# Kernel optimization log

Measured on AMD Instinct MI355X. Metric: run time of the kernel, lower is better.

Reference implementation:

```python
import jax, jax.numpy as jnp
import numpy as np

B, L, D, N, K = 4, 4096, 1024, 64, 3
EPS = 1e-6

def setup_inputs() -> dict:
    key = jax.random.key(0)
    ks = jax.random.split(key, 24)
    f32 = jnp.float32
    inp = {
        'T': jax.random.normal(ks[0], (B, L, D), f32),
        'norm_scale': jnp.ones((D,), f32),
        'in_w': jax.random.normal(ks[1], (2 * D, D), f32) * (1.0 / np.sqrt(D)),
        'in_b': jnp.zeros((2 * D,), f32),
        'dw_w': jax.random.normal(ks[2], (D, 1, K), f32) * (1.0 / np.sqrt(K)),
        'dw_b': jnp.zeros((D,), f32),
        'pw_w': jax.random.normal(ks[3], (D, D), f32) * (1.0 / np.sqrt(D)),
        'pw_b': jnp.zeros((D,), f32),
        'f_win': jax.random.normal(ks[4], (N, D), f32) * (1.0 / np.sqrt(D)),
        'f_wout': jax.random.normal(ks[5], (D, N), f32) * (1.0 / np.sqrt(N)),
        'f_logA': jax.random.normal(ks[6], (N,), f32) * 0.02,
        'f_B': jax.random.normal(ks[7], (N,), f32) * 0.02,
        'f_C': jax.random.normal(ks[8], (N,), f32) * 0.02,
        'f_logdt': jnp.array(0.0, f32),
        'b_win': jax.random.normal(ks[9], (N, D), f32) * (1.0 / np.sqrt(D)),
        'b_wout': jax.random.normal(ks[10], (D, N), f32) * (1.0 / np.sqrt(N)),
        'b_logA': jax.random.normal(ks[11], (N,), f32) * 0.02,
        'b_B': jax.random.normal(ks[12], (N,), f32) * 0.02,
        'b_C': jax.random.normal(ks[13], (N,), f32) * 0.02,
        'b_logdt': jnp.array(0.0, f32),
        'out_w': jax.random.normal(ks[14], (D, D), f32) * (1.0 / np.sqrt(D)),
        'out_b': jnp.zeros((D,), f32),
    }
    return inp

def _ssm(x, win, wout, logA, Bp, Cp, logdt):
    # ZOH discretization of diagonal SSM
    dt = jnp.exp(logdt)
    A = -jnp.exp(logA)
    Abar = jnp.exp(A * dt)
    denom = jnp.where(jnp.abs(A) < EPS, jnp.ones_like(A), A)
    frac = jnp.where(jnp.abs(A) < EPS, dt, (Abar - 1.0) / denom)
    Bbar = frac * Bp
    u = jnp.einsum('bld,nd->bln', x, win)  # (B,L,N)
    h0 = jnp.zeros((x.shape[0], win.shape[0]), x.dtype)
    def step(h, ut):
        h = h * Abar + ut * Bbar
        return h, h * Cp
    _, ys = jax.lax.scan(step, h0, jnp.swapaxes(u, 0, 1))  # (L,B,N)
    y = jnp.swapaxes(ys, 0, 1)
    return jnp.einsum('bln,dn->bld', y, wout)

def reference(T, norm_scale, in_w, in_b, dw_w, dw_b, pw_w, pw_b,
              f_win, f_wout, f_logA, f_B, f_C, f_logdt,
              b_win, b_wout, b_logA, b_B, b_C, b_logdt,
              out_w, out_b):
    # RMSNorm
    rms = jnp.sqrt(jnp.mean(T * T, axis=-1, keepdims=True) + EPS)
    Tn = T / rms * norm_scale
    # in_linear -> chunk
    xz = Tn @ in_w.T + in_b
    x, z = jnp.split(xz, 2, axis=-1)
    gate = jax.nn.sigmoid(z)
    # depthwise-separable conv1d (NCH layout)
    xc = jnp.swapaxes(x, 1, 2)  # (B,D,L)
    xc = jax.lax.conv_general_dilated(
        xc, dw_w, window_strides=(1,), padding=[(K // 2, K // 2)],
        dimension_numbers=('NCH', 'OIH', 'NCH'), feature_group_count=D)
    xc = xc + dw_b[None, :, None]
    xc = jnp.einsum('bdl,ed->bel', xc, pw_w) + pw_b[None, :, None]
    x_conv = jnp.swapaxes(xc, 1, 2)  # (B,L,D)
    # bidirectional SSM
    y_f = _ssm(x_conv, f_win, f_wout, f_logA, f_B, f_C, f_logdt)
    y_b = _ssm(jnp.flip(x_conv, axis=1), b_win, b_wout, b_logA, b_B, b_C, b_logdt)
    y_b = jnp.flip(y_b, axis=1)
    y = (y_f + y_b) * gate
    y = y @ out_w.T + out_b
    return T + y
```

## Files before the change

### kernel.cpp

```cpp
#include <hip/hip_runtime.h>
#include <cstdint>


#define L_SEQ 4096
#define D_DIM 1024
#define B_SZ 4
#define M_TOK (B_SZ * L_SEQ)
#define CHUNKS 64
#define CLEN (L_SEQ / CHUNKS)

typedef short bf16x8 __attribute__((ext_vector_type(8)));
typedef float floatx4 __attribute__((ext_vector_type(4)));

__device__ inline unsigned short f2bf(float f) {
  union { float f; unsigned int u; } v; v.f = f;
  unsigned int r = v.u + 0x7FFFu + ((v.u >> 16) & 1u);
  return (unsigned short)(r >> 16);
}
__device__ inline float bf2f(unsigned short h) {
  union { unsigned int u; float f; } v; v.u = ((unsigned int)h) << 16;
  return v.f;
}

__device__ inline void load_lds16(const unsigned short* g, unsigned short* l) {
  __builtin_amdgcn_global_load_lds(
      (const __attribute__((address_space(1))) unsigned int*)g,
      (__attribute__((address_space(3))) unsigned int*)l, 16, 0, 0);
}

__global__ __launch_bounds__(256) void rmsnorm_kernel(
    const float* __restrict__ T, const float* __restrict__ scale,
    unsigned short* __restrict__ Tn) {
  int tok = blockIdx.x;
  int t = threadIdx.x;
  const float4* row = (const float4*)(T + (size_t)tok * D_DIM);
  float4 v = row[t];
  float ss = v.x*v.x + v.y*v.y + v.z*v.z + v.w*v.w;
  #pragma unroll
  for (int off = 32; off > 0; off >>= 1) ss += __shfl_down(ss, off);
  __shared__ float part[4];
  if ((t & 63) == 0) part[t >> 6] = ss;
  __syncthreads();
  float total = part[0] + part[1] + part[2] + part[3];
  float rinv = rsqrtf(total * (1.0f / D_DIM) + 1e-6f);
  const float4* sc4 = (const float4*)scale;
  float4 s = sc4[t];
  ushort4 o;
  o.x = f2bf(v.x * rinv * s.x); o.y = f2bf(v.y * rinv * s.y);
  o.z = f2bf(v.z * rinv * s.z); o.w = f2bf(v.w * rinv * s.w);
  ((ushort4*)(Tn + (size_t)tok * D_DIM))[t] = o;
}

__global__ __launch_bounds__(256) void f2bf_vec_kernel(
    const float* __restrict__ in, unsigned short* __restrict__ out, int n4) {
  int i = blockIdx.x * 256 + threadIdx.x;
  if (i < n4) {
    float4 v = ((const float4*)in)[i];
    ushort4 o; o.x = f2bf(v.x); o.y = f2bf(v.y); o.z = f2bf(v.z); o.w = f2bf(v.w);
    ((ushort4*)out)[i] = o;
  }
}

__global__ void prepack_kernel(
    const float* __restrict__ f_win, const float* __restrict__ b_win,
    const float* __restrict__ f_wout, const float* __restrict__ b_wout,
    unsigned short* __restrict__ Wu, unsigned short* __restrict__ Wy) {
  int i = blockIdx.x * blockDim.x + threadIdx.x;
  if (i < 128 * D_DIM) {
    int n = i >> 10, k = i & (D_DIM - 1);
    Wu[i] = f2bf((n < 64) ? f_win[n * D_DIM + k] : b_win[(n - 64) * D_DIM + k]);
    int d = i >> 7, kk = i & 127;
    Wy[i] = f2bf((kk < 64) ? f_wout[d * 64 + kk] : b_wout[d * 64 + (kk - 64)]);
  }
}

template<int MODE, typename OUT_T>
__global__ __launch_bounds__(512, 2) void gemm256_kernel(
    const unsigned short* __restrict__ A, const unsigned short* __restrict__ Bw,
    const float* __restrict__ bias, OUT_T* __restrict__ out,
    int M, int N, int Kt,
    const void* __restrict__ aux0, unsigned short* __restrict__ aux1) {
  __shared__ __align__(16) unsigned short As2[2][256 * 64];
  __shared__ __align__(16) unsigned short Bs2[2][256 * 64];
  const int tid = threadIdx.x;
  const int w = tid >> 6, lane = tid & 63;
  const int quad = lane >> 4, lrow = lane & 15;
  const int wm = w >> 2, wn = w & 3;

  const int nx = N >> 8;
  const int nwg = nx * (M >> 8);
  int obid = blockIdx.y * nx + blockIdx.x;
  int swz = (nwg & 7) ? obid : ((obid & 7) * (nwg >> 3) + (obid >> 3));
  const int bm = (swz / nx) << 8;
  const int bn = (swz % nx) << 8;

  const int lr = lane >> 3, ls = lane & 7;
  const int laneOff = lr * Kt + (((ls - lr) & 7) << 3);
  const unsigned short* Asrc = A + (size_t)bm * Kt + laneOff;
  const unsigned short* Bsrc = Bw + (size_t)bn * Kt + laneOff;

  floatx4 acc[8][4] = {};
  const int nkt = Kt >> 6;

  auto stageTile = [&](int buf, int kt) {
    #pragma unroll
    for (int j = 0; j < 4; ++j) {
      int t0 = j * 64 + w * 8;
      load_lds16(Asrc + (size_t)t0 * Kt + kt * 64, &As2[buf][t0 * 64]);
    }
    #pragma unroll
    for (int j = 0; j < 4; ++j) {
      int t0 = j * 64 + w * 8;
      load_lds16(Bsrc + (size_t)t0 * Kt + kt * 64, &Bs2[buf][t0 * 64]);
    }
  };
  auto fragAddr = [&](int r, int ks) {
    return (r << 6) + ((((ks << 2) + quad + r) & 7) << 3);
  };

  const int rA0 = wm * 128 + lrow;
  const int rB0 = wn * 64 + lrow;

  stageTile(0, 0);
  __syncthreads();

  int cur = 0;
  for (int t = 0; t < nkt; ++t) {
    if (t + 1 < nkt) stageTile(cur ^ 1, t + 1);
    const unsigned short* Ab = As2[cur];
    const unsigned short* Bb = Bs2[cur];
    #pragma unroll
    for (int ks = 0; ks < 2; ++ks) {
      bf16x8 af[8], bfr[4];
      #pragma unroll
      for (int mi = 0; mi < 8; ++mi)
        af[mi] = *(const bf16x8*)(Ab + fragAddr(rA0 + mi * 16, ks));
      #pragma unroll
      for (int ni = 0; ni < 4; ++ni)
        bfr[ni] = *(const bf16x8*)(Bb + fragAddr(rB0 + ni * 16, ks));
      __builtin_amdgcn_s_setprio(1);
      #pragma unroll
      for (int mi = 0; mi < 8; ++mi)
        #pragma unroll
        for (int ni = 0; ni < 4; ++ni)
          acc[mi][ni] = __builtin_amdgcn_mfma_f32_16x16x32_bf16(
              af[mi], bfr[ni], acc[mi][ni], 0, 0, 0);
      __builtin_amdgcn_s_setprio(0);
    }
    if (t + 1 < nkt) {
      __syncthreads();
      cur ^= 1;
    }
  }

  #pragma unroll
  for (int mi8 = 0; mi8 < 8; ++mi8) {
    #pragma unroll
    for (int ni = 0; ni < 4; ++ni) {
      #pragma unroll
      for (int r = 0; r < 4; ++r) {
        int m = bm + wm * 128 + mi8 * 16 + quad * 4 + r;
        int n = bn + wn * 64 + ni * 16 + lrow;
        float v = acc[mi8][ni][r];
        if (MODE == 0) {
          if (bias) v += bias[n];
          if (sizeof(OUT_T) == 2) out[(size_t)m * N + n] = (OUT_T)f2bf(v);
          else                    out[(size_t)m * N + n] = (OUT_T)v;
        } else if (MODE == 1) {
          if (bias) v += bias[n];
          if (n < D_DIM) ((unsigned short*)out)[(size_t)m * D_DIM + n] = f2bf(v);
          else aux1[(size_t)m * D_DIM + (n - D_DIM)] = f2bf(1.0f / (1.0f + expf(-v)));
        } else if (MODE == 2) {
          v *= bf2f(((const unsigned short*)aux0)[(size_t)m * N + n]);
          ((unsigned short*)out)[(size_t)m * N + n] = f2bf(v);
        } else {
          if (bias) v += bias[n];
          v += ((const float*)aux0)[(size_t)m * N + n];
          ((float*)out)[(size_t)m * N + n] = v;
        }
      }
    }
  }
}

template<int MODE, typename OUT_T>
__global__ __launch_bounds__(256) void gemm_mfma_kernel(
    const unsigned short* __restrict__ A, const unsigned short* __restrict__ Bw,
    const float* __restrict__ bias, OUT_T* __restrict__ out,
    int M, int N, int Kt,
    const void* __restrict__ aux0, unsigned short* __restrict__ aux1) {
  __shared__ unsigned short As[2][128 * 32];
  __shared__ unsigned short Bs[2][128 * 32];
  int tid = threadIdx.x;
  int wave = tid >> 6, lane = tid & 63;
  int quad = lane >> 4, lrow = lane & 15;
  int bm = blockIdx.y * 128, bn = blockIdx.x * 128;
  int wm = (wave & 1) * 64, wn = (wave >> 1) * 64;

  int r0 = tid >> 2;
  int c8 = (tid & 3) * 8;
  const unsigned short* Ag0 = A  + (size_t)(bm + r0) * Kt + c8;
  const unsigned short* Ag1 = A  + (size_t)(bm + 64 + r0) * Kt + c8;
  const unsigned short* Bg0 = Bw + (size_t)(bn + r0) * Kt + c8;
  const unsigned short* Bg1 = Bw + (size_t)(bn + 64 + r0) * Kt + c8;
  int woff = wave * 512;

  floatx4 acc[4][4] = {};
  int nt = Kt >> 5;

  load_lds16(Ag0, &As[0][0] + woff);
  load_lds16(Ag1, &As[0][0] + 2048 + woff);
  load_lds16(Bg0, &Bs[0][0] + woff);
  load_lds16(Bg1, &Bs[0][0] + 2048 + woff);
  __syncthreads();

  int cur = 0;
  for (int t = 0; t < nt; ++t) {
    if (t + 1 < nt) {
      int k0 = (t + 1) << 5;
      int nb = cur ^ 1;
      load_lds16(Ag0 + k0, &As[nb][0] + woff);
      load_lds16(Ag1 + k0, &As[nb][0] + 2048 + woff);
      load_lds16(Bg0 + k0, &Bs[nb][0] + woff);
      load_lds16(Bg1 + k0, &Bs[nb][0] + 2048 + woff);
    }
    {
      const unsigned short* Ab = &As[cur][0];
      const unsigned short* Bb = &Bs[cur][0];
      bf16x8 af[4], bfr[4];
      #pragma unroll
      for (int mi = 0; mi < 4; ++mi)
        af[mi] = *(const bf16x8*)(Ab + (wm + mi * 16 + lrow) * 32 + quad * 8);
      #pragma unroll
      for (int ni = 0; ni < 4; ++ni)
        bfr[ni] = *(const bf16x8*)(Bb + (wn + ni * 16 + lrow) * 32 + quad * 8);
      __builtin_amdgcn_s_setprio(1);
      #pragma unroll
      for (int mi = 0; mi < 4; ++mi)
        #pragma unroll
        for (int ni = 0; ni < 4; ++ni)
          acc[mi][ni] = __builtin_amdgcn_mfma_f32_16x16x32_bf16(
              af[mi], bfr[ni], acc[mi][ni], 0, 0, 0);
      __builtin_amdgcn_s_setprio(0);
    }
    if (t + 1 < nt) {
      __syncthreads();
      cur ^= 1;
    }
  }

  #pragma unroll
  for (int mi = 0; mi < 4; ++mi) {
    #pragma unroll
    for (int ni = 0; ni < 4; ++ni) {
      #pragma unroll
      for (int r = 0; r < 4; ++r) {
        int m = bm + wm + mi * 16 + quad * 4 + r;
        int n = bn + wn + ni * 16 + lrow;
        float v = acc[mi][ni][r];
        if (MODE == 0) {
          if (bias) v += bias[n];
          if (sizeof(OUT_T) == 2) out[(size_t)m * N + n] = (OUT_T)f2bf(v);
          else                    out[(size_t)m * N + n] = (OUT_T)v;
        } else if (MODE == 1) {
          if (bias) v += bias[n];
          if (n < D_DIM) ((unsigned short*)out)[(size_t)m * D_DIM + n] = f2bf(v);
          else aux1[(size_t)m * D_DIM + (n - D_DIM)] = f2bf(1.0f / (1.0f + expf(-v)));
        } else if (MODE == 2) {
          v *= bf2f(((const unsigned short*)aux0)[(size_t)m * N + n]);
          ((unsigned short*)out)[(size_t)m * N + n] = f2bf(v);
        } else {
          if (bias) v += bias[n];
          v += ((const float*)aux0)[(size_t)m * N + n];
          ((float*)out)[(size_t)m * N + n] = v;
        }
      }
    }
  }
}

__global__ __launch_bounds__(256) void dwconv_kernel(
    const unsigned short* __restrict__ x, const float* __restrict__ w,
    const float* __restrict__ b, unsigned short* __restrict__ out) {
  size_t i8 = (size_t)blockIdx.x * 256 + threadIdx.x;
  int d8 = (int)(i8 & (D_DIM / 8 - 1));
  size_t tok = i8 >> 7;
  int l = (int)(tok & (L_SEQ - 1));
  int d0 = d8 * 8;
  size_t base = tok * D_DIM + d0;
  bf16x8 cur = *(const bf16x8*)(x + base);
  float acc[8];
  #pragma unroll
  for (int j = 0; j < 8; ++j) {
    int d = d0 + j;
    acc[j] = b[d] + w[d * 3 + 1] * bf2f((unsigned short)cur[j]);
  }
  if (l > 0) {
    bf16x8 prv = *(const bf16x8*)(x + base - D_DIM);
    #pragma unroll
    for (int j = 0; j < 8; ++j) acc[j] += w[(d0 + j) * 3 + 0] * bf2f((unsigned short)prv[j]);
  }
  if (l < L_SEQ - 1) {
    bf16x8 nxt = *(const bf16x8*)(x + base + D_DIM);
    #pragma unroll
    for (int j = 0; j < 8; ++j) acc[j] += w[(d0 + j) * 3 + 2] * bf2f((unsigned short)nxt[j]);
  }
  bf16x8 o;
  #pragma unroll
  for (int j = 0; j < 8; ++j) o[j] = (short)f2bf(acc[j]);
  *(bf16x8*)(out + base) = o;
}

__device__ inline void ssm_params(
    int col,
    const float* f_logA, const float* f_B, const float* f_C, const float* f_logdt,
    const float* b_logA, const float* b_B, const float* b_C, const float* b_logdt,
    float& Abar, float& Bbar, float& Cc, float& Aa, float& dt) {
  int dir = col >> 6, n = col & 63;
  const float* logA  = dir ? b_logA  : f_logA;
  const float* Bp    = dir ? b_B     : f_B;
  const float* Cp    = dir ? b_C     : f_C;
  const float* logdt = dir ? b_logdt : f_logdt;
  dt = expf(logdt[0]);
  Aa = -expf(logA[n]);
  Abar = expf(Aa * dt);
  float frac = (fabsf(Aa) < 1e-6f) ? dt : (Abar - 1.0f) / Aa;
  Bbar = frac * Bp[n];
  Cc = Cp[n];
}

__global__ __launch_bounds__(128) void scan_s1_kernel(
    const float* __restrict__ u, float* __restrict__ states,
    const float* __restrict__ f_logA, const float* __restrict__ f_B,
    const float* __restrict__ f_C, const float* __restrict__ f_logdt,
    const float* __restrict__ b_logA, const float* __restrict__ b_B,
    const float* __restrict__ b_C, const float* __restrict__ b_logdt) {
  int col = threadIdx.x;
  int chunk = blockIdx.x, b = blockIdx.y;
  float Abar, Bbar, Cc, Aa, dt;
  ssm_params(col, f_logA, f_B, f_C, f_logdt, b_logA, b_B, b_C, b_logdt,
             Abar, Bbar, Cc, Aa, dt);
  size_t base = ((size_t)b * L_SEQ + (size_t)chunk * CLEN) * 128 + col;
  float h = 0.0f;
  if (col < 64) {
    for (int i0 = 0; i0 < CLEN; i0 += 8) {
      float uv[8];
      #pragma unroll
      for (int j = 0; j < 8; ++j) uv[j] = u[base + (size_t)(i0 + j) * 128];
      #pragma unroll
      for (int j = 0; j < 8; ++j) h = h * Abar + uv[j] * Bbar;
    }
  } else {
    for (int i0 = CLEN - 1; i0 >= 0; i0 -= 8) {
      float uv[8];
      #pragma unroll
      for (int j = 0; j < 8; ++j) uv[j] = u[base + (size_t)(i0 - j) * 128];
      #pragma unroll
      for (int j = 0; j < 8; ++j) h = h * Abar + uv[j] * Bbar;
    }
  }
  states[((size_t)b * CHUNKS + chunk) * 128 + col] = h;
}

__global__ __launch_bounds__(512) void scan_s2_kernel(
    const float* __restrict__ states, float* __restrict__ carries,
    const float* __restrict__ f_logA, const float* __restrict__ f_B,
    const float* __restrict__ f_C, const float* __restrict__ f_logdt,
    const float* __restrict__ b_logA, const float* __restrict__ b_B,
    const float* __restrict__ b_C, const float* __restrict__ b_logdt) {
  int tid = threadIdx.x;
  int b = tid >> 7, col = tid & 127;
  float Abar, Bbar, Cc, Aa, dt;
  ssm_params(col, f_logA, f_B, f_C, f_logdt, b_logA, b_B, b_C, b_logdt,
             Abar, Bbar, Cc, Aa, dt);
  float Ac = expf(Aa * dt * (float)CLEN);
  size_t sb = (size_t)b * CHUNKS * 128 + col;
  float cur = 0.0f;
  if (col < 64) {
    for (int c = 0; c < CHUNKS; ++c) {
      carries[sb + (size_t)c * 128] = cur;
      cur = cur * Ac + states[sb + (size_t)c * 128];
    }
  } else {
    for (int c = CHUNKS - 1; c >= 0; --c) {
      carries[sb + (size_t)c * 128] = cur;
      cur = cur * Ac + states[sb + (size_t)c * 128];
    }
  }
}

__global__ __launch_bounds__(128) void scan_s3_kernel(
    const float* __restrict__ u, const float* __restrict__ carries,
    unsigned short* __restrict__ y,
    const float* __restrict__ f_logA, const float* __restrict__ f_B,
    const float* __restrict__ f_C, const float* __restrict__ f_logdt,
    const float* __restrict__ b_logA, const float* __restrict__ b_B,
    const float* __restrict__ b_C, const float* __restrict__ b_logdt) {
  int col = threadIdx.x;
  int chunk = blockIdx.x, b = blockIdx.y;
  float Abar, Bbar, Cc, Aa, dt;
  ssm_params(col, f_logA, f_B, f_C, f_logdt, b_logA, b_B, b_C, b_logdt,
             Abar, Bbar, Cc, Aa, dt);
  size_t base = ((size_t)b * L_SEQ + (size_t)chunk * CLEN) * 128 + col;
  float h = carries[((size_t)b * CHUNKS + chunk) * 128 + col];
  if (col < 64) {
    for (int i0 = 0; i0 < CLEN; i0 += 8) {
      float uv[8];
      #pragma unroll
      for (int j = 0; j < 8; ++j) uv[j] = u[base + (size_t)(i0 + j) * 128];
      #pragma unroll
      for (int j = 0; j < 8; ++j) {
        h = h * Abar + uv[j] * Bbar;
        y[base + (size_t)(i0 + j) * 128] = f2bf(h * Cc);
      }
    }
  } else {
    for (int i0 = CLEN - 1; i0 >= 0; i0 -= 8) {
      float uv[8];
      #pragma unroll
      for (int j = 0; j < 8; ++j) uv[j] = u[base + (size_t)(i0 - j) * 128];
      #pragma unroll
      for (int j = 0; j < 8; ++j) {
        h = h * Abar + uv[j] * Bbar;
        y[base + (size_t)(i0 - j) * 128] = f2bf(h * Cc);
      }
    }
  }
}

extern "C" void kernel_launch(void* const* d_in, const int* in_sizes, int n_in,
                              void* d_out, int out_size, void* d_ws, size_t ws_size,
                              hipStream_t stream) {
  const float* T         = (const float*)d_in[0];
  const float* norm_scale= (const float*)d_in[1];
  const float* in_w      = (const float*)d_in[2];
  const float* in_b      = (const float*)d_in[3];
  const float* dw_w      = (const float*)d_in[4];
  const float* dw_b      = (const float*)d_in[5];
  const float* pw_w      = (const float*)d_in[6];
  const float* pw_b      = (const float*)d_in[7];
  const float* f_win     = (const float*)d_in[8];
  const float* f_wout    = (const float*)d_in[9];
  const float* f_logA    = (const float*)d_in[10];
  const float* f_B       = (const float*)d_in[11];
  const float* f_C       = (const float*)d_in[12];
  const float* f_logdt   = (const float*)d_in[13];
  const float* b_win     = (const float*)d_in[14];
  const float* b_wout    = (const float*)d_in[15];
  const float* b_logA    = (const float*)d_in[16];
  const float* b_B       = (const float*)d_in[17];
  const float* b_C       = (const float*)d_in[18];
  const float* b_logdt   = (const float*)d_in[19];
  const float* out_w     = (const float*)d_in[20];
  const float* out_b     = (const float*)d_in[21];
  float* out = (float*)d_out;

  char* ws = (char*)d_ws;
  const size_t MD = (size_t)M_TOK * D_DIM;
  unsigned short* gate  = (unsigned short*)ws;              ws += MD * 2;
  unsigned short* bufA  = (unsigned short*)ws;              ws += MD * 2;
  unsigned short* bufB  = (unsigned short*)ws;              ws += MD * 2;
  float*          u     = (float*)ws;                       ws += (size_t)M_TOK * 128 * 4;
  unsigned short* ybuf  = (unsigned short*)ws;              ws += (size_t)M_TOK * 128 * 2;
  unsigned short* w_in  = (unsigned short*)ws;              ws += (size_t)2 * D_DIM * D_DIM * 2;
  unsigned short* w_pw  = (unsigned short*)ws;              ws += (size_t)D_DIM * D_DIM * 2;
  unsigned short* w_out = (unsigned short*)ws;              ws += (size_t)D_DIM * D_DIM * 2;
  unsigned short* Wu    = (unsigned short*)ws;              ws += (size_t)128 * D_DIM * 2;
  unsigned short* Wy    = (unsigned short*)ws;              ws += (size_t)128 * D_DIM * 2;
  float*          states= (float*)ws;                       ws += (size_t)B_SZ * CHUNKS * 128 * 4;
  float*          carries=(float*)ws;

  f2bf_vec_kernel<<<(2 * D_DIM * D_DIM / 4 + 255) / 256, 256, 0, stream>>>(in_w, w_in, 2 * D_DIM * D_DIM / 4);
  f2bf_vec_kernel<<<(D_DIM * D_DIM / 4 + 255) / 256, 256, 0, stream>>>(pw_w, w_pw, D_DIM * D_DIM / 4);
  f2bf_vec_kernel<<<(D_DIM * D_DIM / 4 + 255) / 256, 256, 0, stream>>>(out_w, w_out, D_DIM * D_DIM / 4);
  prepack_kernel<<<(128 * D_DIM) / 256, 256, 0, stream>>>(f_win, b_win, f_wout, b_wout, Wu, Wy);
  rmsnorm_kernel<<<M_TOK, 256, 0, stream>>>(T, norm_scale, bufA);
  {
    dim3 g((2 * D_DIM) / 256, M_TOK / 256);
    gemm256_kernel<1, unsigned short><<<g, 512, 0, stream>>>(
        bufA, w_in, in_b, bufB, M_TOK, 2 * D_DIM, D_DIM, nullptr, gate);
  }
  dwconv_kernel<<<(MD / 8) / 256, 256, 0, stream>>>(bufB, dw_w, dw_b, bufA);
  {
    dim3 g(D_DIM / 256, M_TOK / 256);
    gemm256_kernel<0, unsigned short><<<g, 512, 0, stream>>>(
        bufA, w_pw, pw_b, bufB, M_TOK, D_DIM, D_DIM, nullptr, nullptr);
  }
  {
    dim3 g(1, M_TOK / 128);
    gemm_mfma_kernel<0, float><<<g, 256, 0, stream>>>(
        bufB, Wu, nullptr, u, M_TOK, 128, D_DIM, nullptr, nullptr);
  }
  {
    dim3 g1(CHUNKS, B_SZ);
    scan_s1_kernel<<<g1, 128, 0, stream>>>(u, states, f_logA, f_B, f_C, f_logdt,
                                           b_logA, b_B, b_C, b_logdt);
    scan_s2_kernel<<<1, 512, 0, stream>>>(states, carries, f_logA, f_B, f_C, f_logdt,
                                          b_logA, b_B, b_C, b_logdt);
    scan_s3_kernel<<<g1, 128, 0, stream>>>(u, carries, ybuf, f_logA, f_B, f_C, f_logdt,
                                           b_logA, b_B, b_C, b_logdt);
  }
  {
    dim3 g(D_DIM / 256, M_TOK / 256);
    gemm256_kernel<2, unsigned short><<<g, 512, 0, stream>>>(
        ybuf, Wy, nullptr, bufA, M_TOK, D_DIM, 128, gate, nullptr);
  }
  {
    dim3 g(D_DIM / 256, M_TOK / 256);
    gemm256_kernel<3, float><<<g, 512, 0, stream>>>(
        bufA, w_out, out_b, out, M_TOK, D_DIM, D_DIM, T, nullptr);
  }
}
```

Baseline: 674.6 us.

## Restructure GEMM main loop into register-double-buffered pipeline with explicit waitcnts

Replaces the simple LDS double-buffer loop with an unrolled two-tile loop that prefetches both tiles up front, splits each K tile into two half-steps with fragment registers double-buffered, and uses explicit vmcnt/lgkmcnt waits plus raw barriers so global loads for the next tile are issued early and overlap MFMA work. The aim is to hide LDS-read and global-load latency behind matrix math and cut full __syncthreads stalls. It relies on hand-tuned vmcnt counts tied to the number of loads per stage and assumes nkt is even, and the extra fragment registers raise register pressure under a 512-thread, two-block launch bound.

```diff
diff --git a/kernel.cpp b/kernel.cpp
--- a/kernel.cpp
+++ b/kernel.cpp
@@ -80,8 +80,10 @@
     const float* __restrict__ bias, OUT_T* __restrict__ out,
     int M, int N, int Kt,
     const void* __restrict__ aux0, unsigned short* __restrict__ aux1) {
-  __shared__ __align__(16) unsigned short As2[2][256 * 64];
-  __shared__ __align__(16) unsigned short Bs2[2][256 * 64];
+  __shared__ __align__(16) unsigned short As0[256 * 64];
+  __shared__ __align__(16) unsigned short As1[256 * 64];
+  __shared__ __align__(16) unsigned short Bs0[256 * 64];
+  __shared__ __align__(16) unsigned short Bs1[256 * 64];
   const int tid = threadIdx.x;
   const int w = tid >> 6, lane = tid & 63;
   const int quad = lane >> 4, lrow = lane & 15;
@@ -102,56 +104,76 @@
   floatx4 acc[8][4] = {};
   const int nkt = Kt >> 6;
 
-  auto stageTile = [&](int buf, int kt) {
-    #pragma unroll
-    for (int j = 0; j < 4; ++j) {
-      int t0 = j * 64 + w * 8;
-      load_lds16(Asrc + (size_t)t0 * Kt + kt * 64, &As2[buf][t0 * 64]);
-    }
-    #pragma unroll
-    for (int j = 0; j < 4; ++j) {
-      int t0 = j * 64 + w * 8;
-      load_lds16(Bsrc + (size_t)t0 * Kt + kt * 64, &Bs2[buf][t0 * 64]);
-    }
-  };
+#define STAGE_TILE(AS, BS, KT) do {                                          \
+    _Pragma("unroll")                                                        \
+    for (int j = 0; j < 4; ++j) {                                            \
+      int t0 = j * 64 + w * 8;                                               \
+      load_lds16(Asrc + (size_t)t0 * Kt + (size_t)(KT) * 64, &AS[t0 * 64]);  \
+    }                                                                        \
+    _Pragma("unroll")                                                        \
+    for (int j = 0; j < 4; ++j) {                                            \
+      int t0 = j * 64 + w * 8;                                               \
+      load_lds16(Bsrc + (size_t)t0 * Kt + (size_t)(KT) * 64, &BS[t0 * 64]);  \
+    }                                                                        \
+  } while (0)
+
   auto fragAddr = [&](int r, int ks) {
     return (r << 6) + ((((ks << 2) + quad + r) & 7) << 3);
   };
-
   const int rA0 = wm * 128 + lrow;
   const int rB0 = wn * 64 + lrow;
 
-  stageTile(0, 0);
-  __syncthreads();
-
-  int cur = 0;
-  for (int t = 0; t < nkt; ++t) {
-    if (t + 1 < nkt) stageTile(cur ^ 1, t + 1);
-    const unsigned short* Ab = As2[cur];
-    const unsigned short* Bb = Bs2[cur];
-    #pragma unroll
-    for (int ks = 0; ks < 2; ++ks) {
-      bf16x8 af[8], bfr[4];
-      #pragma unroll
-      for (int mi = 0; mi < 8; ++mi)
-        af[mi] = *(const bf16x8*)(Ab + fragAddr(rA0 + mi * 16, ks));
-      #pragma unroll
-      for (int ni = 0; ni < 4; ++ni)
-        bfr[ni] = *(const bf16x8*)(Bb + fragAddr(rB0 + ni * 16, ks));
-      __builtin_amdgcn_s_setprio(1);
-      #pragma unroll
-      for (int mi = 0; mi < 8; ++mi)
-        #pragma unroll
-        for (int ni = 0; ni < 4; ++ni)
-          acc[mi][ni] = __builtin_amdgcn_mfma_f32_16x16x32_bf16(
-              af[mi], bfr[ni], acc[mi][ni], 0, 0, 0);
-      __builtin_amdgcn_s_setprio(0);
-    }
-    if (t + 1 < nkt) {
-      __syncthreads();
-      cur ^= 1;
-    }
-  }
+#define READ_FRAGS(AS, BS, KS, AF, BF) do {                                  \
+    _Pragma("unroll")                                                        \
+    for (int mi = 0; mi < 8; ++mi)                                           \
+      AF[mi] = *(const bf16x8*)(AS + fragAddr(rA0 + mi * 16, KS));           \
+    _Pragma("unroll")                                                        \
+    for (int ni = 0; ni < 4; ++ni)                                           \
+      BF[ni] = *(const bf16x8*)(BS + fragAddr(rB0 + ni * 16, KS));           \
+  } while (0)
+
+#define MFMA_BLOCK(AF, BF) do {                                              \
+    __builtin_amdgcn_s_setprio(1);                                           \
+    _Pragma("unroll")                                                        \
+    for (int mi = 0; mi < 8; ++mi)                                           \
+      _Pragma("unroll")                                                      \
+      for (int ni = 0; ni < 4; ++ni)                                         \
+        acc[mi][ni] = __builtin_amdgcn_mfma_f32_16x16x32_bf16(               \
+            AF[mi], BF[ni], acc[mi][ni], 0, 0, 0);                           \
+    __builtin_amdgcn_s_setprio(0);                                           \
+  } while (0)
+
+  STAGE_TILE(As0, Bs0, 0);
+  STAGE_TILE(As1, Bs1, 1);
+
+  bf16x8 afA[8], bfA[4], afB[8], bfB[4];
+  const int nIter = nkt >> 1;
+  for (int i = 0; i < nIter; ++i) {
+    asm volatile("s_waitcnt vmcnt(8)" ::: "memory");
+    __builtin_amdgcn_s_barrier();
+    READ_FRAGS(As0, Bs0, 0, afA, bfA);
+    MFMA_BLOCK(afA, bfA);
+    READ_FRAGS(As0, Bs0, 1, afB, bfB);
+    asm volatile("s_waitcnt lgkmcnt(0)" ::: "memory");
+    __builtin_amdgcn_s_barrier();
+    if (2 * i + 2 < nkt) STAGE_TILE(As0, Bs0, 2 * i + 2);
+    MFMA_BLOCK(afB, bfB);
+    if (2 * i + 2 < nkt)
+      asm volatile("s_waitcnt vmcnt(8)" ::: "memory");
+    else
+      asm volatile("s_waitcnt vmcnt(0)" ::: "memory");
+    __builtin_amdgcn_s_barrier();
+    READ_FRAGS(As1, Bs1, 0, afA, bfA);
+    MFMA_BLOCK(afA, bfA);
+    READ_FRAGS(As1, Bs1, 1, afB, bfB);
+    asm volatile("s_waitcnt lgkmcnt(0)" ::: "memory");
+    __builtin_amdgcn_s_barrier();
+    if (2 * i + 3 < nkt) STAGE_TILE(As1, Bs1, 2 * i + 3);
+    MFMA_BLOCK(afB, bfB);
+  }
+#undef STAGE_TILE
+#undef READ_FRAGS
+#undef MFMA_BLOCK
 
   #pragma unroll
   for (int mi8 = 0; mi8 < 8; ++mi8) {
```

Result: slower. 1.115 ms (+65.3%).
